# Kernel optimization log

Hardware: AMD Instinct MI355X
Metric: run time of the kernel (lower is better)

Reference implementation:

```python
import jax, jax.numpy as jnp
import numpy as np

T = 8           # hardcoded frame count in forward
MAX_D = 3       # hardcoded displacement radius -> 7x7 = 49-entry cost volume
PATCH = 2 * MAX_D + 1
EPS = 1e-12     # F.normalize eps


def _l2norm_c(x):
    # x: [B, C, H, W]; L2-normalize over channel dim (torch F.normalize dim=1)
    n = jnp.sqrt(jnp.sum(x * x, axis=1, keepdims=True))
    return x / jnp.maximum(n, EPS)


def setup_inputs() -> dict:
    key = jax.random.key(0)
    ks = jax.random.split(key, 6)
    B, N, C = 2, 8192, 512
    nh = 8
    d = C // nh
    return {
        "x": jax.random.normal(ks[0], (B, N, C), jnp.float32),
        "w_qk": jax.random.normal(ks[1], (2 * C, C), jnp.float32) * 0.02,
        "w_corr": jax.random.normal(ks[2], (d, PATCH * PATCH), jnp.float32) * 0.02,
        "b_corr": jax.random.normal(ks[3], (d,), jnp.float32) * 0.02,
        "w_proj": jax.random.normal(ks[4], (C, C), jnp.float32) * 0.02,
        "b_proj": jax.random.normal(ks[5], (C,), jnp.float32) * 0.02,
    }


def reference(x, w_qk, w_corr, b_corr, w_proj, b_proj):
    B, N, C = x.shape
    nh = 8
    d = C // nh
    H = int(round((N // T) ** 0.5))
    W = H

    # qk projection (no bias): [B, N, 2C] -> [2, B, nh, N, d]
    qk = jnp.einsum('bnc,ec->bne', x, w_qk).reshape(B, N, 2, nh, d)
    q = jnp.transpose(qk[:, :, 0], (0, 2, 1, 3))  # [B, nh, N, d]
    k = jnp.transpose(qk[:, :, 1], (0, 2, 1, 3))

    # 'b n (t h w) d -> (b n) t d h w'
    def to_vid(a):
        a = a.reshape(B, nh, T, H, W, d)
        return jnp.transpose(a, (0, 1, 2, 5, 3, 4)).reshape(B * nh, T, d, H, W)

    q = to_vid(q)
    k = to_vid(k)

    # k_postfix: shift time forward, repeat last frame
    k_post = jnp.concatenate([k[:, 1:], k[:, -1:]], axis=1)

    BT = B * nh * T
    qf = _l2norm_c(q.reshape(BT, d, H, W))
    kf = _l2norm_c(k_post.reshape(BT, d, H, W))

    # local cost volume: corr[b, u*7+v, y, x] = sum_c qf[b,c,y,x] * kf[b,c,y+u-3,x+v-3]
    kp = jnp.pad(kf, ((0, 0), (0, 0), (MAX_D, MAX_D), (MAX_D, MAX_D)))
    corr = jnp.stack(
        [jnp.sum(qf * kp[:, :, u:u + H, v:v + W], axis=1)
         for u in range(PATCH) for v in range(PATCH)],
        axis=1,
    )  # [BT, 49, H, W]

    # 'b u v h w -> b (h w) (u v)'
    corr = jnp.transpose(corr, (0, 2, 3, 1)).reshape(BT, H * W, PATCH * PATCH)

    # proj_corr: 49 -> head_dim
    mf = jnp.einsum('bpk,dk->bpd', corr, w_corr) + b_corr  # [BT, HW, d]

    # '(b n t) (h w) d -> b (t h w) (n d)'
    mf = mf.reshape(B, nh, T, H, W, d)
    mf = jnp.transpose(mf, (0, 2, 3, 4, 1, 5)).reshape(B, N, C)

    # final projection
    return jnp.einsum('bnc,oc->bno', mf, w_proj) + b_proj
```

## Files before the change

kernel.cpp:

```cpp
#include <hip/hip_runtime.h>

typedef unsigned int u32;
typedef unsigned short u16;
typedef __fp16 h2 __attribute__((ext_vector_type(2)));
typedef __fp16 f16x8 __attribute__((ext_vector_type(8)));
typedef float f32x4 __attribute__((ext_vector_type(4)));

#define DEVFN static __device__ __forceinline__

DEVFN u32 pkh(float a, float b) {
  return __builtin_bit_cast(u32, __builtin_amdgcn_cvt_pkrtz(a, b));
}
DEVFN u16 f2h(float f) { __fp16 h = (__fp16)f; return __builtin_bit_cast(u16, h); }

#if __has_builtin(__builtin_amdgcn_fdot2)
DEVFN float dot2u(u32 a, u32 b, float c) {
  return __builtin_amdgcn_fdot2(__builtin_bit_cast(h2, a),
                                __builtin_bit_cast(h2, b), c, false);
}
#else
DEVFN float dot2u(u32 a, u32 b, float c) {
  h2 x = __builtin_bit_cast(h2, a), y = __builtin_bit_cast(h2, b);
  return c + (float)x[0] * (float)y[0] + (float)x[1] * (float)y[1];
}
#endif

DEVFN uint4 pk8(f32x4 lo, f32x4 hi) {
  uint4 o;
  o.x = pkh(lo.x, lo.y); o.y = pkh(lo.z, lo.w);
  o.z = pkh(hi.x, hi.y); o.w = pkh(hi.z, hi.w);
  return o;
}

template <int MODE, int F32, int TN>
__global__ __launch_bounds__(256) void gemm(
    const void* __restrict__ A_, const void* __restrict__ B_,
    const float* __restrict__ bias, void* __restrict__ Out_,
    int Nn, int K) {
  __shared__ u16 As[2][4096];
  __shared__ u16 Bs[2][4096];
  const int tid = threadIdx.x;
  const int lane = tid & 63;
  const int w = tid >> 6;
  const int wm = w >> 1, wn = w & 1;
  const int nwg = (int)gridDim.x;
  const int wg = ((int)blockIdx.x & 7) * (nwg >> 3) + ((int)blockIdx.x >> 3);
  const int tm = wg / TN, tn = wg % TN;

  const float* Af = (const float*)A_;
  const float* Bf = (const float*)B_;
  const u16* Ah = (const u16*)A_;
  const u16* Bh = (const u16*)B_;

  const int rr = tid >> 2;
  const int s8 = (tid & 3) << 3;
  const size_t offA = (size_t)(tm * 128 + rr) * K + s8;
  const size_t offB = (size_t)(tn * 128 + rr) * K + s8;
  const int wofs = rr * 32 + s8;

  const int rofsA = ((wm * 64 + (lane & 15)) << 5) + ((lane >> 4) << 3);
  const int rofsB = ((wn * 64 + (lane & 15)) << 5) + ((lane >> 4) << 3);

  f32x4 acc[4][4] = {};
  const int KT = K >> 5;

  f32x4 a0, a1, a2, a3, b0, b1, b2, b3;
  uint4 ha0, ha1, hb0, hb1;

#define ISSUE(t)                                                          \
  {                                                                       \
    const size_t oa = offA + (size_t)(t) * 32;                            \
    const size_t ob = offB + (size_t)(t) * 32;                            \
    if (F32) {                                                            \
      a0 = *(const f32x4*)(Af + oa);                                      \
      a1 = *(const f32x4*)(Af + oa + 4);                                  \
      a2 = *(const f32x4*)(Af + oa + (size_t)64 * K);                     \
      a3 = *(const f32x4*)(Af + oa + (size_t)64 * K + 4);                 \
      b0 = *(const f32x4*)(Bf + ob);                                      \
      b1 = *(const f32x4*)(Bf + ob + 4);                                  \
      b2 = *(const f32x4*)(Bf + ob + (size_t)64 * K);                     \
      b3 = *(const f32x4*)(Bf + ob + (size_t)64 * K + 4);                 \
    } else {                                                              \
      ha0 = *(const uint4*)(Ah + oa);                                     \
      ha1 = *(const uint4*)(Ah + oa + (size_t)64 * K);                    \
      hb0 = *(const uint4*)(Bh + ob);                                     \
      hb1 = *(const uint4*)(Bh + ob + (size_t)64 * K);                    \
    }                                                                     \
  }

#define WRITE(bufi)                                                       \
  {                                                                       \
    u16* da = &As[bufi][wofs];                                            \
    u16* db = &Bs[bufi][wofs];                                            \
    if (F32) {                                                            \
      *(uint4*)da = pk8(a0, a1);                                          \
      *(uint4*)(da + 2048) = pk8(a2, a3);                                 \
      *(uint4*)db = pk8(b0, b1);                                          \
      *(uint4*)(db + 2048) = pk8(b2, b3);                                 \
    } else {                                                              \
      *(uint4*)da = ha0;                                                  \
      *(uint4*)(da + 2048) = ha1;                                         \
      *(uint4*)db = hb0;                                                  \
      *(uint4*)(db + 2048) = hb1;                                         \
    }                                                                     \
  }

  ISSUE(0)
  WRITE(0)
  ISSUE(1)
  __syncthreads();

  for (int kt = 0; kt < KT; ++kt) {
    const int cur = kt & 1;
    if (kt + 1 < KT) {
      WRITE(cur ^ 1)
      if (kt + 2 < KT) ISSUE(kt + 2)
    }
    f16x8 af[4], bf[4];
#pragma unroll
    for (int i = 0; i < 4; ++i) af[i] = *(const f16x8*)(&As[cur][rofsA + i * 512]);
#pragma unroll
    for (int i = 0; i < 4; ++i) bf[i] = *(const f16x8*)(&Bs[cur][rofsB + i * 512]);
#pragma unroll
    for (int mi = 0; mi < 4; ++mi)
#pragma unroll
      for (int ni = 0; ni < 4; ++ni)
        acc[mi][ni] = __builtin_amdgcn_mfma_f32_16x16x32_f16(af[mi], bf[ni],
                                                             acc[mi][ni], 0, 0, 0);
    __syncthreads();
  }
#undef ISSUE
#undef WRITE

  const int rowBase = tm * 128 + wm * 64 + ((lane >> 4) << 2);
  const int colBase = tn * 128 + wn * 64 + (lane & 15);

  if (MODE == 1) {
    float* Out = (float*)Out_;
    float bv[4];
#pragma unroll
    for (int ni = 0; ni < 4; ++ni) bv[ni] = bias[colBase + ni * 16];
#pragma unroll
    for (int mi = 0; mi < 4; ++mi)
#pragma unroll
      for (int r = 0; r < 4; ++r) {
        size_t ro = (size_t)(rowBase + mi * 16 + r) * Nn;
#pragma unroll
        for (int ni = 0; ni < 4; ++ni)
          Out[ro + colBase + ni * 16] = acc[mi][ni][r] + bv[ni];
      }
  } else {
    u16* Out = (u16*)Out_;
    const int sel = colBase >> 9;
    const int hh = (colBase >> 6) & 7;
    const int ddb = lane & 15;
#pragma unroll
    for (int mi = 0; mi < 4; ++mi)
#pragma unroll
      for (int r = 0; r < 4; ++r) {
        float s = acc[mi][0][r] * acc[mi][0][r] + acc[mi][1][r] * acc[mi][1][r] +
                  acc[mi][2][r] * acc[mi][2][r] + acc[mi][3][r] * acc[mi][3][r];
        s += __shfl_xor(s, 1);
        s += __shfl_xor(s, 2);
        s += __shfl_xor(s, 4);
        s += __shfl_xor(s, 8);
        float inv = 1.0f / fmaxf(sqrtf(s), 1e-12f);
        const int m = rowBase + mi * 16 + r;
        const int bb = m >> 13, tt = (m >> 10) & 7, pix = m & 1023;
        const int fr = ((sel * 2 + bb) * 8 + tt) * 8 + hh;
        size_t base = (((size_t)fr) << 16) + (size_t)pix * 64 + ddb;
#pragma unroll
        for (int ni = 0; ni < 4; ++ni)
          Out[base + ni * 16] = f2h(acc[mi][ni][r] * inv);
      }
  }
}

__global__ __launch_bounds__(256) void dots_w2(
    const u16* __restrict__ qf, u16* __restrict__ corr,
    const float* __restrict__ wp, const float* __restrict__ wc,
    const float* __restrict__ bc, const float* __restrict__ bp,
    u16* __restrict__ W2, float* __restrict__ cvec) {
  __shared__ __align__(16) u16 smem[448 * 64];
  const int tid = threadIdx.x;

  if ((int)blockIdx.x >= 512) {
    const int o = (int)blockIdx.x - 512;
    float* wcl = (float*)smem;
    float* wpl = wcl + 3136;
    for (int i = tid; i < 3136; i += 256) wcl[i] = wc[i];
    wpl[tid] = wp[o * 512 + tid];
    wpl[tid + 256] = wp[o * 512 + tid + 256];
    __syncthreads();
#pragma unroll
    for (int pass = 0; pass < 2; ++pass) {
      const int idx = pass * 256 + tid;
      const int hh = idx >> 6, r = idx & 63, du = r >> 3, dv = r & 7;
      float sv = 0.f;
      if (du < 7 && dv < 7) {
#pragma unroll
        for (int c = 0; c < 64; ++c)
          sv += wpl[hh * 64 + c] * wcl[c * 49 + du * 7 + dv];
      }
      W2[o * 512 + idx] = f2h(sv);
    }
    if (tid < 64) {
      float p = 0.f;
#pragma unroll
      for (int g = 0; g < 8; ++g) p += wpl[g * 64 + tid];
      p *= bc[tid];
      p += __shfl_xor(p, 1); p += __shfl_xor(p, 2); p += __shfl_xor(p, 4);
      p += __shfl_xor(p, 8); p += __shfl_xor(p, 16); p += __shfl_xor(p, 32);
      if (tid == 0) cvec[o] = p + bp[o];
    }
    return;
  }

  u16* kst = smem;
  const int bid = ((int)blockIdx.x & 7) * 64 + ((int)blockIdx.x >> 3);
  const int fr = bid >> 2, grp = bid & 3;
  const int h = fr & 7, t = (fr >> 3) & 7, b = fr >> 6;
  const int t1 = (t < 7) ? t + 1 : 7;
  const int y0 = grp * 8;

  const u16* kbase = qf + (((size_t)(((2 + b) * 8 + t1) * 8 + h)) << 16);
  {
    const int ppx = tid >> 3;
    const int slot = tid & 7;
#pragma unroll
    for (int pass = 0; pass < 14; ++pass) {
      int gy = y0 - 3 + pass;
      uint4 v = make_uint4(0, 0, 0, 0);
      if ((unsigned)gy < 32u)
        v = *(const uint4*)(kbase + (size_t)(gy * 32 + ppx) * 64 + slot * 8);
      int pl = pass * 32 + ppx;
      *(uint4*)((char*)kst + pl * 128 + ((slot * 16) ^ ((pl & 7) << 4))) = v;
    }
  }

  const int px = grp * 256 + tid;
  const int x = tid & 31, yloc = tid >> 5;
  const u16* qp = qf + (((size_t)fr) << 16) + (size_t)px * 64;
  u32 qw[32];
#pragma unroll
  for (int j = 0; j < 8; ++j) {
    uint4 v = *(const uint4*)(qp + j * 8);
    qw[j * 4 + 0] = v.x; qw[j * 4 + 1] = v.y;
    qw[j * 4 + 2] = v.z; qw[j * 4 + 3] = v.w;
  }
  __syncthreads();

  u16* mp = corr + (size_t)((b * 8 + t) * 1024 + px) * 512 + h * 64;
  for (int du = 0; du < 7; ++du) {
    const int rlbase = (yloc + du) * 32;
    float f[7];
#pragma unroll
    for (int dv = 0; dv < 7; ++dv) {
      int xx = x + dv - 3;
      int xc = xx < 0 ? 0 : (xx > 31 ? 31 : xx);
      int pl = rlbase + xc;
      const char* kr = (const char*)kst + pl * 128;
      const int swz = (pl & 7) << 4;
      float s0 = 0.f, s1 = 0.f, s2 = 0.f, s3 = 0.f;
#pragma unroll
      for (int j = 0; j < 8; ++j) {
        uint4 v = *(const uint4*)(kr + ((j * 16) ^ swz));
        s0 = dot2u(qw[j * 4 + 0], v.x, s0);
        s1 = dot2u(qw[j * 4 + 1], v.y, s1);
        s2 = dot2u(qw[j * 4 + 2], v.z, s2);
        s3 = dot2u(qw[j * 4 + 3], v.w, s3);
      }
      float s = (s0 + s1) + (s2 + s3);
      f[dv] = ((unsigned)xx < 32u) ? s : 0.f;
    }
    uint4 o;
    o.x = pkh(f[0], f[1]); o.y = pkh(f[2], f[3]);
    o.z = pkh(f[4], f[5]); o.w = pkh(f[6], 0.f);
    *(uint4*)(mp + du * 8) = o;
  }
  *(uint4*)(mp + 56) = make_uint4(0, 0, 0, 0);
}

extern "C" void kernel_launch(void* const* d_in, const int* in_sizes, int n_in,
                              void* d_out, int out_size, void* d_ws, size_t ws_size,
                              hipStream_t stream) {
  const float* x      = (const float*)d_in[0];
  const float* w_qk   = (const float*)d_in[1];
  const float* w_corr = (const float*)d_in[2];
  const float* b_corr = (const float*)d_in[3];
  const float* w_proj = (const float*)d_in[4];
  const float* b_proj = (const float*)d_in[5];
  float* out = (float*)d_out;

  u16* corr = (u16*)d_ws;
  u16* qf   = corr + (size_t)16384 * 512;
  u16* W2   = qf + (size_t)16384 * 1024;
  float* cvec = (float*)(W2 + (size_t)512 * 512);

  gemm<0, 1, 8><<<dim3(1024), dim3(256), 0, stream>>>(
      x, w_qk, nullptr, qf, 1024, 512);
  dots_w2<<<dim3(1024), dim3(256), 0, stream>>>(qf, corr, w_proj, w_corr,
                                                b_corr, b_proj, W2, cvec);
  gemm<1, 0, 4><<<dim3(512), dim3(256), 0, stream>>>(
      corr, W2, cvec, out, 512, 512);
}
```

Measured before the change: 79.47 us.

## Use direct global-to-LDS loads for fp16 GEMM staging with raw barriers

For the fp16-input GEMM path, global loads now go directly into LDS via global_load_lds instead of passing through registers, with explicit vmcnt waits and raw s_barrier. The fp32 path reorders LDS fragment reads before the next tile's write. MFMA blocks are wrapped in s_setprio to favour math waves. The aim is to cut register pressure and VGPR round-trips for staging and overlap loads with MFMA, at the risk of LDS layout mismatches or sync hazards with the hand-written waits.

```diff
diff --git a/kernel.cpp b/kernel.cpp
--- a/kernel.cpp
+++ b/kernel.cpp
@@ -30,6 +30,20 @@
   o.x = pkh(lo.x, lo.y); o.y = pkh(lo.z, lo.w);
   o.z = pkh(hi.x, hi.y); o.w = pkh(hi.z, hi.w);
   return o;
+}
+
+DEVFN void gld16(const u16* g, u16* l) {
+  __builtin_amdgcn_global_load_lds(
+      (const __attribute__((address_space(1))) u32*)g,
+      (__attribute__((address_space(3))) u32*)l, 16, 0, 0);
+}
+
+DEVFN void waitv0() { asm volatile("s_waitcnt vmcnt(0)" ::: "memory"); }
+DEVFN void waitl0() { asm volatile("s_waitcnt lgkmcnt(0)" ::: "memory"); }
+DEVFN void rbar() {
+  __builtin_amdgcn_sched_barrier(0);
+  __builtin_amdgcn_s_barrier();
+  __builtin_amdgcn_sched_barrier(0);
 }
 
 template <int MODE, int F32, int TN>
@@ -58,6 +72,11 @@
   const size_t offB = (size_t)(tn * 128 + rr) * K + s8;
   const int wofs = rr * 32 + s8;
 
+  const int sr = w * 32 + (lane >> 2);
+  const int sc = (lane & 3) << 3;
+  const u16* gA = Ah + (size_t)(tm * 128 + sr) * K + sc;
+  const u16* gB = Bh + (size_t)(tn * 128 + sr) * K + sc;
+
   const int rofsA = ((wm * 64 + (lane & 15)) << 5) + ((lane >> 4) << 3);
   const int rofsB = ((wn * 64 + (lane & 15)) << 5) + ((lane >> 4) << 3);
 
@@ -65,72 +84,82 @@
   const int KT = K >> 5;
 
   f32x4 a0, a1, a2, a3, b0, b1, b2, b3;
-  uint4 ha0, ha1, hb0, hb1;
-
-#define ISSUE(t)                                                          \
+
+#define LOADF(t)                                                          \
   {                                                                       \
     const size_t oa = offA + (size_t)(t) * 32;                            \
     const size_t ob = offB + (size_t)(t) * 32;                            \
-    if (F32) {                                                            \
-      a0 = *(const f32x4*)(Af + oa);                                      \
-      a1 = *(const f32x4*)(Af + oa + 4);                                  \
-      a2 = *(const f32x4*)(Af + oa + (size_t)64 * K);                     \
-      a3 = *(const f32x4*)(Af + oa + (size_t)64 * K + 4);                 \
-      b0 = *(const f32x4*)(Bf + ob);                                      \
-      b1 = *(const f32x4*)(Bf + ob + 4);                                  \
-      b2 = *(const f32x4*)(Bf + ob + (size_t)64 * K);                     \
-      b3 = *(const f32x4*)(Bf + ob + (size_t)64 * K + 4);                 \
-    } else {                                                              \
-      ha0 = *(const uint4*)(Ah + oa);                                     \
-      ha1 = *(const uint4*)(Ah + oa + (size_t)64 * K);                    \
-      hb0 = *(const uint4*)(Bh + ob);                                     \
-      hb1 = *(const uint4*)(Bh + ob + (size_t)64 * K);                    \
-    }                                                                     \
-  }
-
-#define WRITE(bufi)                                                       \
+    a0 = *(const f32x4*)(Af + oa);                                        \
+    a1 = *(const f32x4*)(Af + oa + 4);                                    \
+    a2 = *(const f32x4*)(Af + oa + (size_t)64 * K);                       \
+    a3 = *(const f32x4*)(Af + oa + (size_t)64 * K + 4);                   \
+    b0 = *(const f32x4*)(Bf + ob);                                        \
+    b1 = *(const f32x4*)(Bf + ob + 4);                                    \
+    b2 = *(const f32x4*)(Bf + ob + (size_t)64 * K);                       \
+    b3 = *(const f32x4*)(Bf + ob + (size_t)64 * K + 4);                   \
+  }
+#define WRITEF(bufi)                                                      \
   {                                                                       \
     u16* da = &As[bufi][wofs];                                            \
     u16* db = &Bs[bufi][wofs];                                            \
-    if (F32) {                                                            \
-      *(uint4*)da = pk8(a0, a1);                                          \
-      *(uint4*)(da + 2048) = pk8(a2, a3);                                 \
-      *(uint4*)db = pk8(b0, b1);                                          \
-      *(uint4*)(db + 2048) = pk8(b2, b3);                                 \
-    } else {                                                              \
-      *(uint4*)da = ha0;                                                  \
-      *(uint4*)(da + 2048) = ha1;                                         \
-      *(uint4*)db = hb0;                                                  \
-      *(uint4*)(db + 2048) = hb1;                                         \
-    }                                                                     \
-  }
-
-  ISSUE(0)
-  WRITE(0)
-  ISSUE(1)
-  __syncthreads();
+    *(uint4*)da = pk8(a0, a1);                                            \
+    *(uint4*)(da + 2048) = pk8(a2, a3);                                   \
+    *(uint4*)db = pk8(b0, b1);                                            \
+    *(uint4*)(db + 2048) = pk8(b2, b3);                                   \
+  }
+#define STAGEH(bufi, t)                                                   \
+  {                                                                       \
+    gld16(gA + (size_t)(t) * 32, &As[bufi][w * 1024]);                    \
+    gld16(gA + (size_t)(t) * 32 + (size_t)16 * K, &As[bufi][w * 1024 + 512]); \
+    gld16(gB + (size_t)(t) * 32, &Bs[bufi][w * 1024]);                    \
+    gld16(gB + (size_t)(t) * 32 + (size_t)16 * K, &Bs[bufi][w * 1024 + 512]); \
+  }
+
+  if (F32) {
+    LOADF(0)
+    WRITEF(0)
+    LOADF(1)
+    waitl0();
+  } else {
+    STAGEH(0, 0)
+    waitv0();
+  }
+  rbar();
 
   for (int kt = 0; kt < KT; ++kt) {
     const int cur = kt & 1;
-    if (kt + 1 < KT) {
-      WRITE(cur ^ 1)
-      if (kt + 2 < KT) ISSUE(kt + 2)
-    }
     f16x8 af[4], bf[4];
-#pragma unroll
-    for (int i = 0; i < 4; ++i) af[i] = *(const f16x8*)(&As[cur][rofsA + i * 512]);
-#pragma unroll
-    for (int i = 0; i < 4; ++i) bf[i] = *(const f16x8*)(&Bs[cur][rofsB + i * 512]);
+    if (F32) {
+#pragma unroll
+      for (int i = 0; i < 4; ++i) af[i] = *(const f16x8*)(&As[cur][rofsA + i * 512]);
+#pragma unroll
+      for (int i = 0; i < 4; ++i) bf[i] = *(const f16x8*)(&Bs[cur][rofsB + i * 512]);
+      if (kt + 1 < KT) {
+        WRITEF(cur ^ 1)
+        if (kt + 2 < KT) LOADF(kt + 2)
+      }
+    } else {
+      if (kt + 1 < KT) STAGEH(cur ^ 1, kt + 1)
+#pragma unroll
+      for (int i = 0; i < 4; ++i) af[i] = *(const f16x8*)(&As[cur][rofsA + i * 512]);
+#pragma unroll
+      for (int i = 0; i < 4; ++i) bf[i] = *(const f16x8*)(&Bs[cur][rofsB + i * 512]);
+    }
+    __builtin_amdgcn_s_setprio(1);
 #pragma unroll
     for (int mi = 0; mi < 4; ++mi)
 #pragma unroll
       for (int ni = 0; ni < 4; ++ni)
         acc[mi][ni] = __builtin_amdgcn_mfma_f32_16x16x32_f16(af[mi], bf[ni],
                                                              acc[mi][ni], 0, 0, 0);
-    __syncthreads();
-  }
-#undef ISSUE
-#undef WRITE
+    __builtin_amdgcn_s_setprio(0);
+    if (F32) waitl0();
+    else waitv0();
+    rbar();
+  }
+#undef LOADF
+#undef WRITEF
+#undef STAGEH
 
   const int rowBase = tm * 128 + wm * 64 + ((lane >> 4) << 2);
   const int colBase = tn * 128 + wn * 64 + (lane & 15);
```

Result: no change. 78.89 us (-0.7%).

## Load GEMM B operand directly into registers, bypassing shared memory

Applied to the files above, without the earlier changes.

The B tile is no longer staged through LDS. Each wave loads its own B fragments straight from global memory into registers, in MFMA layout, one k-step ahead, and only A goes through double-buffered shared memory. The barrier is replaced with an explicit lgkmcnt wait plus a raw s_barrier, and MFMA issue priority is raised. This cuts LDS traffic and capacity, but B rows are now read redundantly by the waves sharing a column and register pressure rises. It also relies on the barrier ordering global-load consumption correctly, since vmcnt is not waited on explicitly.

```diff
diff --git a/kernel.cpp b/kernel.cpp
--- a/kernel.cpp
+++ b/kernel.cpp
@@ -30,6 +30,14 @@
   o.x = pkh(lo.x, lo.y); o.y = pkh(lo.z, lo.w);
   o.z = pkh(hi.x, hi.y); o.w = pkh(hi.z, hi.w);
   return o;
+}
+DEVFN f16x8 h8(uint4 v) { return __builtin_bit_cast(f16x8, v); }
+
+DEVFN void waitl0() { asm volatile("s_waitcnt lgkmcnt(0)" ::: "memory"); }
+DEVFN void rbar() {
+  __builtin_amdgcn_sched_barrier(0);
+  __builtin_amdgcn_s_barrier();
+  __builtin_amdgcn_sched_barrier(0);
 }
 
 template <int MODE, int F32, int TN>
@@ -38,7 +46,6 @@
     const float* __restrict__ bias, void* __restrict__ Out_,
     int Nn, int K) {
   __shared__ u16 As[2][4096];
-  __shared__ u16 Bs[2][4096];
   const int tid = threadIdx.x;
   const int lane = tid & 63;
   const int w = tid >> 6;
@@ -55,82 +62,102 @@
   const int rr = tid >> 2;
   const int s8 = (tid & 3) << 3;
   const size_t offA = (size_t)(tm * 128 + rr) * K + s8;
-  const size_t offB = (size_t)(tn * 128 + rr) * K + s8;
   const int wofs = rr * 32 + s8;
 
+  const size_t offB = (size_t)(tn * 128 + wn * 64 + (lane & 15)) * K +
+                      ((lane >> 4) << 3);
+
   const int rofsA = ((wm * 64 + (lane & 15)) << 5) + ((lane >> 4) << 3);
-  const int rofsB = ((wn * 64 + (lane & 15)) << 5) + ((lane >> 4) << 3);
 
   f32x4 acc[4][4] = {};
   const int KT = K >> 5;
 
-  f32x4 a0, a1, a2, a3, b0, b1, b2, b3;
-  uint4 ha0, ha1, hb0, hb1;
-
-#define ISSUE(t)                                                          \
+  f32x4 fa0, fa1, fa2, fa3;
+  uint4 ua0, ua1;
+  f32x4 pb[8];
+  uint4 ub[4];
+
+#define LOADB(t)                                                          \
+  {                                                                       \
+    const size_t ob = offB + (size_t)(t) * 32;                            \
+    if (F32) {                                                            \
+      _Pragma("unroll") for (int ni = 0; ni < 4; ++ni) {                  \
+        pb[2 * ni] = *(const f32x4*)(Bf + ob + (size_t)16 * ni * K);      \
+        pb[2 * ni + 1] = *(const f32x4*)(Bf + ob + (size_t)16 * ni * K + 4); \
+      }                                                                   \
+    } else {                                                              \
+      _Pragma("unroll") for (int ni = 0; ni < 4; ++ni)                    \
+        ub[ni] = *(const uint4*)(Bh + ob + (size_t)16 * ni * K);          \
+    }                                                                     \
+  }
+#define CVTB(bf)                                                          \
+  {                                                                       \
+    if (F32) {                                                            \
+      _Pragma("unroll") for (int ni = 0; ni < 4; ++ni)                    \
+        bf[ni] = h8(pk8(pb[2 * ni], pb[2 * ni + 1]));                     \
+    } else {                                                              \
+      _Pragma("unroll") for (int ni = 0; ni < 4; ++ni) bf[ni] = h8(ub[ni]); \
+    }                                                                     \
+  }
+#define LOADA(t)                                                          \
   {                                                                       \
     const size_t oa = offA + (size_t)(t) * 32;                            \
-    const size_t ob = offB + (size_t)(t) * 32;                            \
     if (F32) {                                                            \
-      a0 = *(const f32x4*)(Af + oa);                                      \
-      a1 = *(const f32x4*)(Af + oa + 4);                                  \
-      a2 = *(const f32x4*)(Af + oa + (size_t)64 * K);                     \
-      a3 = *(const f32x4*)(Af + oa + (size_t)64 * K + 4);                 \
-      b0 = *(const f32x4*)(Bf + ob);                                      \
-      b1 = *(const f32x4*)(Bf + ob + 4);                                  \
-      b2 = *(const f32x4*)(Bf + ob + (size_t)64 * K);                     \
-      b3 = *(const f32x4*)(Bf + ob + (size_t)64 * K + 4);                 \
+      fa0 = *(const f32x4*)(Af + oa);                                     \
+      fa1 = *(const f32x4*)(Af + oa + 4);                                 \
+      fa2 = *(const f32x4*)(Af + oa + (size_t)64 * K);                    \
+      fa3 = *(const f32x4*)(Af + oa + (size_t)64 * K + 4);                \
     } else {                                                              \
-      ha0 = *(const uint4*)(Ah + oa);                                     \
-      ha1 = *(const uint4*)(Ah + oa + (size_t)64 * K);                    \
-      hb0 = *(const uint4*)(Bh + ob);                                     \
-      hb1 = *(const uint4*)(Bh + ob + (size_t)64 * K);                    \
+      ua0 = *(const uint4*)(Ah + oa);                                     \
+      ua1 = *(const uint4*)(Ah + oa + (size_t)64 * K);                    \
     }                                                                     \
   }
-
-#define WRITE(bufi)                                                       \
+#define WRITEA(bufi)                                                      \
   {                                                                       \
     u16* da = &As[bufi][wofs];                                            \
-    u16* db = &Bs[bufi][wofs];                                            \
     if (F32) {                                                            \
-      *(uint4*)da = pk8(a0, a1);                                          \
-      *(uint4*)(da + 2048) = pk8(a2, a3);                                 \
-      *(uint4*)db = pk8(b0, b1);                                          \
-      *(uint4*)(db + 2048) = pk8(b2, b3);                                 \
+      *(uint4*)da = pk8(fa0, fa1);                                        \
+      *(uint4*)(da + 2048) = pk8(fa2, fa3);                               \
     } else {                                                              \
-      *(uint4*)da = ha0;                                                  \
-      *(uint4*)(da + 2048) = ha1;                                         \
-      *(uint4*)db = hb0;                                                  \
-      *(uint4*)(db + 2048) = hb1;                                         \
+      *(uint4*)da = ua0;                                                  \
+      *(uint4*)(da + 2048) = ua1;                                         \
     }                                                                     \
   }
 
-  ISSUE(0)
-  WRITE(0)
-  ISSUE(1)
-  __syncthreads();
+  LOADA(0)
+  WRITEA(0)
+  LOADB(0)
+  LOADA(1)
+  waitl0();
+  rbar();
 
   for (int kt = 0; kt < KT; ++kt) {
     const int cur = kt & 1;
+    f16x8 bf[4];
+    CVTB(bf)
+    f16x8 af[4];
+#pragma unroll
+    for (int i = 0; i < 4; ++i) af[i] = *(const f16x8*)(&As[cur][rofsA + i * 512]);
     if (kt + 1 < KT) {
-      WRITE(cur ^ 1)
-      if (kt + 2 < KT) ISSUE(kt + 2)
-    }
-    f16x8 af[4], bf[4];
-#pragma unroll
-    for (int i = 0; i < 4; ++i) af[i] = *(const f16x8*)(&As[cur][rofsA + i * 512]);
-#pragma unroll
-    for (int i = 0; i < 4; ++i) bf[i] = *(const f16x8*)(&Bs[cur][rofsB + i * 512]);
+      WRITEA(cur ^ 1)
+      LOADB(kt + 1)
+      if (kt + 2 < KT) LOADA(kt + 2)
+    }
+    __builtin_amdgcn_s_setprio(1);
 #pragma unroll
     for (int mi = 0; mi < 4; ++mi)
 #pragma unroll
       for (int ni = 0; ni < 4; ++ni)
         acc[mi][ni] = __builtin_amdgcn_mfma_f32_16x16x32_f16(af[mi], bf[ni],
                                                              acc[mi][ni], 0, 0, 0);
-    __syncthreads();
-  }
-#undef ISSUE
-#undef WRITE
+    __builtin_amdgcn_s_setprio(0);
+    waitl0();
+    rbar();
+  }
+#undef LOADB
+#undef CVTB
+#undef LOADA
+#undef WRITEA
 
   const int rowBase = tm * 128 + wm * 64 + ((lane >> 4) << 2);
   const int colBase = tn * 128 + wn * 64 + (lane & 15);
```

New measurement: 124.6 us. 56.8% more time.
